# Performance work log

Hardware: AMD Instinct MI355X
Metric: run time of the kernel (lower is better)

## Reference

```python
import jax, jax.numpy as jnp
import numpy as np

N, K, H = 100000, 16, 128


def setup_inputs() -> dict:
    key = jax.random.key(0)
    ks = jax.random.split(key, 9)
    return {
        "p_init": jax.random.normal(ks[0], (N,), dtype=jnp.float32),
        "r_matrix": jax.random.normal(ks[1], (N, K, 5), dtype=jnp.float32),
        "w1": jax.random.normal(ks[2], (1 + 5, H), dtype=jnp.float32) * 0.1,
        "b1": jax.random.normal(ks[3], (H,), dtype=jnp.float32) * 0.1,
        "w2": jax.random.normal(ks[4], (H + 5, H), dtype=jnp.float32) * 0.05,
        "b2": jax.random.normal(ks[5], (H,), dtype=jnp.float32) * 0.05,
        "w3": jax.random.normal(ks[6], (H + 5, 1), dtype=jnp.float32) * 0.05,
        "b3": jax.random.normal(ks[7], (1,), dtype=jnp.float32) * 0.05,
        "indices_neigh_tri": jax.random.randint(ks[8], (N, K + 1), 0, N, dtype=jnp.int64),
    }


def _stage(f, neigh, r_matrix, w, b):
    # f: [N, C]; neigh: [N, K]; r_matrix: [N, K, 5]
    diff = f[:, None, :] - f[neigh]                      # [N, K, C]
    r_diff = jnp.concatenate([r_matrix, diff], axis=2)   # [N, K, 5+C]
    out = jnp.einsum('nkc,co->nko', r_diff, w) + b       # [N, K, O]
    return out.sum(axis=1)                               # [N, O]


def reference(p_init, r_matrix, w1, b1, w2, b2, w3, b3, indices_neigh_tri):
    neigh = indices_neigh_tri[:, 1:]                     # [N, K]
    f = p_init[:, None]                                  # [N, 1]
    f = jax.nn.relu(_stage(f, neigh, r_matrix, w1, b1))  # [N, H]
    f = jax.nn.relu(_stage(f, neigh, r_matrix, w2, b2))  # [N, H]
    logits = _stage(f, neigh, r_matrix, w3, b3).squeeze(-1)  # [N]
    return jax.nn.softmax(logits, axis=0)
```

## Files before the change

### kernel.cpp

```cpp
#include <hip/hip_runtime.h>
#include <hip/hip_bf16.h>
#include <hip/hip_fp16.h>


#define NN 100000
#define KK 16
#define HH 128

typedef _Float16 half8 __attribute__((ext_vector_type(8)));
typedef float f32x4 __attribute__((ext_vector_type(4)));
typedef float f32x2 __attribute__((ext_vector_type(2)));

__global__ __launch_bounds__(256) void prep_kernel(
    const float* __restrict__ p, const float* __restrict__ rmat,
    const int* __restrict__ idx, float* __restrict__ vv,
    unsigned int* __restrict__ gmk, float* __restrict__ pstot) {
  const int tid = threadIdx.x;
  if (blockIdx.x == 0 && tid == 0) { gmk[0] = 0u; pstot[0] = 0.f; }
  const int sub = tid & 3;
  const int n = blockIdx.x * 64 + (tid >> 2);
  if (n >= NN) return;
  const float4* rr = (const float4*)(rmat) + (size_t)n * 20;
  float t[5] = {0.f, 0.f, 0.f, 0.f, 0.f};
#pragma unroll
  for (int j = 0; j < 5; ++j) {
    const float4 q = rr[sub + 4 * j];
    t[(j + 0) % 5] += q.x;
    t[(j + 1) % 5] += q.y;
    t[(j + 2) % 5] += q.z;
    t[(j + 3) % 5] += q.w;
  }
  float rs[5];
#pragma unroll
  for (int c = 0; c < 5; ++c) {
    float v = t[c];
    v = (sub == 1) ? t[(c + 1) % 5] : v;
    v = (sub == 2) ? t[(c + 2) % 5] : v;
    v = (sub == 3) ? t[(c + 3) % 5] : v;
    rs[c] = v;
  }
  const int* nb = idx + (size_t)n * 17 + 1;
  float ps = 0.f;
#pragma unroll
  for (int k = 0; k < 4; ++k) ps += p[nb[sub * 4 + k]];
#pragma unroll
  for (int c = 0; c < 5; ++c) {
    rs[c] += __shfl_xor(rs[c], 1, 64);
    rs[c] += __shfl_xor(rs[c], 2, 64);
  }
  ps += __shfl_xor(ps, 1, 64);
  ps += __shfl_xor(ps, 2, 64);
  if (sub == 0) {
    float4 lo; lo.x = rs[0]; lo.y = rs[1]; lo.z = rs[2]; lo.w = rs[3];
    *(float4*)&vv[(size_t)n * 8] = lo;
  } else if (sub == 1) {
    float4 hi; hi.x = rs[4]; hi.y = 16.f * p[n] - ps; hi.z = 0.f; hi.w = 0.f;
    *(float4*)&vv[(size_t)n * 8 + 4] = hi;
  }
}

__global__ __launch_bounds__(256, 2) void gemm2_kernel(
    const float* __restrict__ vv, const float* __restrict__ w1,
    const float* __restrict__ b1, const float* __restrict__ w2,
    unsigned char* __restrict__ A8) {
  __shared__ __align__(16) _Float16 s_w1[6][128];
  __shared__ __align__(16) _Float16 s_b1[128];
  const int tid = threadIdx.x;
  if (tid < 128) {
#pragma unroll
    for (int c = 0; c < 6; ++c) s_w1[c][tid] = (_Float16)w1[c * HH + tid];
    s_b1[tid] = (_Float16)(16.f * b1[tid]);
  }
  const int lane = tid & 63;
  const int wgl = (blockIdx.x << 2) + (tid >> 6);
  const int colhalf = wgl & 1;
  const int strip0 = wgl >> 1;
  const int sstride = (gridDim.x << 2) >> 1;
  const int r16 = lane & 15;
  const int g16 = lane >> 4;

  half8 wfrag[4][4];
#pragma unroll
  for (int ct = 0; ct < 4; ++ct) {
#pragma unroll
    for (int kk = 0; kk < 4; ++kk) {
      const int hcol = colhalf * 64 + ct * 16 + r16;
#pragma unroll
      for (int e = 0; e < 8; ++e)
        wfrag[ct][kk][e] = (_Float16)w2[(size_t)(5 + kk * 32 + g16 * 8 + e) * HH + hcol];
    }
  }
  __syncthreads();

  for (int strip = strip0; strip < NN / 16; strip += sstride) {
    const int nbase = strip * 16;
    const float* vr = vv + (size_t)(nbase + r16) * 8;
    const float4 vlo = *(const float4*)vr;
    const float4 vhi = *(const float4*)(vr + 4);
    const _Float16 x0 = (_Float16)vlo.x, x1 = (_Float16)vlo.y,
                   x2 = (_Float16)vlo.z, x3 = (_Float16)vlo.w,
                   x4 = (_Float16)vhi.x, x5 = (_Float16)vhi.y;
    half8 xfrag[4];
#pragma unroll
    for (int kk = 0; kk < 4; ++kk) {
      const int off = kk * 32 + g16 * 8;
      half8 a = *(const half8*)&s_b1[off];
      const half8 w0 = *(const half8*)&s_w1[0][off];
      const half8 w1v = *(const half8*)&s_w1[1][off];
      const half8 w2v = *(const half8*)&s_w1[2][off];
      const half8 w3v = *(const half8*)&s_w1[3][off];
      const half8 w4v = *(const half8*)&s_w1[4][off];
      const half8 w5v = *(const half8*)&s_w1[5][off];
#pragma unroll
      for (int e = 0; e < 8; ++e) {
        _Float16 v = a[e] + w0[e] * x0 + w1v[e] * x1 + w2v[e] * x2
                   + w3v[e] * x3 + w4v[e] * x4 + w5v[e] * x5;
        a[e] = v > (_Float16)0.f ? v : (_Float16)0.f;
      }
      xfrag[kk] = a;
    }
    f32x4 acc[4] = {{0.f,0.f,0.f,0.f},{0.f,0.f,0.f,0.f},{0.f,0.f,0.f,0.f},{0.f,0.f,0.f,0.f}};
#pragma unroll
    for (int kk = 0; kk < 4; ++kk) {
#pragma unroll
      for (int ct = 0; ct < 4; ++ct)
        acc[ct] = __builtin_amdgcn_mfma_f32_16x16x32_f16(wfrag[ct][kk], xfrag[kk], acc[ct], 0, 0, 0);
    }
#pragma unroll
    for (int ct = 0; ct < 4; ++ct) {
      int packed = __builtin_amdgcn_cvt_pk_fp8_f32(acc[ct][0], acc[ct][1], 0, false);
      packed = __builtin_amdgcn_cvt_pk_fp8_f32(acc[ct][2], acc[ct][3], packed, true);
      *(int*)&A8[(size_t)(nbase + r16) * HH + colhalf * 64 + ct * 16 + g16 * 4] = packed;
    }
  }
}

#define REDUCE_PAIR(NBASE, AV0, AV1, DRAW)                                    \
  {                                                                           \
    f32x2 s0l = {0.f,0.f}, s0h = {0.f,0.f}, s1l = {0.f,0.f}, s1h = {0.f,0.f};\
    _Pragma("unroll")                                                         \
    for (int pp = 0; pp < 8; ++pp) {                                          \
      s0l -= __builtin_amdgcn_cvt_pk_f32_fp8(AV0[pp], false);                 \
      s0h -= __builtin_amdgcn_cvt_pk_f32_fp8(AV0[pp], true);                  \
      s1l -= __builtin_amdgcn_cvt_pk_f32_fp8(AV1[pp], false);                 \
      s1h -= __builtin_amdgcn_cvt_pk_f32_fp8(AV1[pp], true);                  \
    }                                                                         \
    {                                                                         \
      const int nd = (NBASE) + half;                                          \
      f32x2 dl = b2l + __builtin_amdgcn_cvt_pk_f32_fp8(DRAW, false);          \
      f32x2 dh = b2h + __builtin_amdgcn_cvt_pk_f32_fp8(DRAW, true);           \
      dl *= 16.f; dh *= 16.f;                                                 \
      const float* vr = vv + (size_t)nd * 8;                                  \
      _Pragma("unroll")                                                       \
      for (int j = 0; j < 5; ++j) {                                           \
        const float r = vr[j];                                                \
        dl += r * w2rl[j]; dh += r * w2rh[j];                                 \
      }                                                                       \
      if (half == 0) { s0l += dl; s0h += dh; }                                \
      else           { s1l += dl; s1h += dh; }                                \
    }                                                                         \
    s0l[0] += __shfl_xor(s0l[0], 32, 64); s0l[1] += __shfl_xor(s0l[1], 32, 64);\
    s0h[0] += __shfl_xor(s0h[0], 32, 64); s0h[1] += __shfl_xor(s0h[1], 32, 64);\
    s1l[0] += __shfl_xor(s1l[0], 32, 64); s1l[1] += __shfl_xor(s1l[1], 32, 64);\
    s1h[0] += __shfl_xor(s1h[0], 32, 64); s1h[1] += __shfl_xor(s1h[1], 32, 64);\
    float v0 = fmaxf(s0l[0], 0.f) * w3l[0] + fmaxf(s0l[1], 0.f) * w3l[1]      \
             + fmaxf(s0h[0], 0.f) * w3h[0] + fmaxf(s0h[1], 0.f) * w3h[1];     \
    float v1 = fmaxf(s1l[0], 0.f) * w3l[0] + fmaxf(s1l[1], 0.f) * w3l[1]      \
             + fmaxf(s1h[0], 0.f) * w3h[0] + fmaxf(s1h[1], 0.f) * w3h[1];     \
    _Pragma("unroll")                                                         \
    for (int off = 16; off > 0; off >>= 1) {                                  \
      v0 += __shfl_xor(v0, off, 64);                                          \
      v1 += __shfl_xor(v1, off, 64);                                          \
    }                                                                         \
    if (lane == 0) { sv[(NBASE)] = v0; sv[(NBASE) + 1] = v1; }                \
  }

__global__ __launch_bounds__(256) void gather2_kernel(
    const unsigned char* __restrict__ A8, const float* __restrict__ vv,
    const float* __restrict__ w2, const float* __restrict__ b2,
    const float* __restrict__ w3, const int* __restrict__ idx,
    float* __restrict__ sv) {
  const int lane = threadIdx.x & 63;
  const int half = lane >> 5;
  const int q = lane & 31;
  const int wid = (blockIdx.x << 2) + (threadIdx.x >> 6);
  const int nwaves = gridDim.x << 2;
  const f32x2 w3l = {w3[5 + 4 * q], w3[6 + 4 * q]};
  const f32x2 w3h = {w3[7 + 4 * q], w3[8 + 4 * q]};
  f32x2 w2rl[5], w2rh[5];
#pragma unroll
  for (int j = 0; j < 5; ++j) {
    w2rl[j] = *(const f32x2*)&w2[j * 128 + (q << 2)];
    w2rh[j] = *(const f32x2*)&w2[j * 128 + (q << 2) + 2];
  }
  const f32x2 b2l = *(const f32x2*)&b2[(q << 2)];
  const f32x2 b2h = *(const f32x2*)&b2[(q << 2) + 2];

  for (int t = wid; t < NN / 4; t += nwaves) {
    const int n = t * 4;
    const int* nb = idx + (size_t)n * 17 + 1;
    unsigned int avA[8], avB[8], avC[8], avD[8];
#pragma unroll
    for (int pp = 0; pp < 8; ++pp) {
      const int k = 2 * pp + half;
      avA[pp] = *(const unsigned int*)&A8[(size_t)nb[k]      * HH + (q << 2)];
      avB[pp] = *(const unsigned int*)&A8[(size_t)nb[17 + k] * HH + (q << 2)];
    }
    const unsigned int dAB = *(const unsigned int*)&A8[(size_t)(n + half) * HH + (q << 2)];
#pragma unroll
    for (int pp = 0; pp < 8; ++pp) {
      const int k = 2 * pp + half;
      avC[pp] = *(const unsigned int*)&A8[(size_t)nb[34 + k] * HH + (q << 2)];
      avD[pp] = *(const unsigned int*)&A8[(size_t)nb[51 + k] * HH + (q << 2)];
    }
    const unsigned int dCD = *(const unsigned int*)&A8[(size_t)(n + 2 + half) * HH + (q << 2)];
    REDUCE_PAIR(n, avA, avB, dAB)
    REDUCE_PAIR(n + 2, avC, avD, dCD)
  }
}

__device__ __forceinline__ unsigned int fkey(float f) {
  unsigned int b = __float_as_uint(f);
  return (b & 0x80000000u) ? ~b : (b | 0x80000000u);
}

__global__ __launch_bounds__(256) void stage3s_kernel(
    const float* __restrict__ sv, const float* __restrict__ vv,
    const float* __restrict__ w3, const float* __restrict__ b3,
    const int* __restrict__ idx, float* __restrict__ lg,
    unsigned int* __restrict__ gmk) {
  __shared__ float s[256];
  const int n = blockIdx.x * 256 + threadIdx.x;
  float t = -3.4e38f;
  if (n < NN) {
    t = 16.f * sv[n];
    const int* nb = idx + (size_t)n * 17 + 1;
#pragma unroll
    for (int k = 0; k < KK; ++k) t -= sv[nb[k]];
#pragma unroll
    for (int c = 0; c < 5; ++c) t += vv[(size_t)n * 8 + c] * w3[c];
    t += 16.f * b3[0];
    lg[n] = t;
  }
  s[threadIdx.x] = t; __syncthreads();
  for (int off = 128; off > 0; off >>= 1) {
    if (threadIdx.x < off) s[threadIdx.x] = fmaxf(s[threadIdx.x], s[threadIdx.x + off]);
    __syncthreads();
  }
  if (threadIdx.x == 0) atomicMax(gmk, fkey(s[0]));
}

__global__ __launch_bounds__(256) void expsum_kernel(
    const float* __restrict__ lg, const unsigned int* __restrict__ gmk,
    float* __restrict__ out, float* __restrict__ pstot) {
  __shared__ float s[256];
  const int tid = threadIdx.x;
  const unsigned int k = gmk[0];
  const float m = __uint_as_float((k & 0x80000000u) ? (k & 0x7FFFFFFFu) : ~k);
  float acc = 0.f;
  for (int i = blockIdx.x * 256 + tid; i < NN; i += 256 * 256) {
    float e = __expf(lg[i] - m);
    out[i] = e;
    acc += e;
  }
  s[tid] = acc; __syncthreads();
  for (int off = 128; off > 0; off >>= 1) {
    if (tid < off) s[tid] += s[tid + off];
    __syncthreads();
  }
  if (tid == 0) atomicAdd(pstot, s[0]);
}

__global__ __launch_bounds__(256) void scale_kernel(
    float* __restrict__ out, const float* __restrict__ pstot) {
  const int i = blockIdx.x * 256 + threadIdx.x;
  const float inv = 1.f / pstot[0];
  if (i < NN) out[i] *= inv;
}

extern "C" void kernel_launch(void* const* d_in, const int* in_sizes, int n_in,
                              void* d_out, int out_size, void* d_ws, size_t ws_size,
                              hipStream_t stream) {
  const float* p    = (const float*)d_in[0];
  const float* rmat = (const float*)d_in[1];
  const float* w1   = (const float*)d_in[2];
  const float* b1   = (const float*)d_in[3];
  const float* w2   = (const float*)d_in[4];
  const float* b2   = (const float*)d_in[5];
  const float* w3   = (const float*)d_in[6];
  const float* b3   = (const float*)d_in[7];
  const int*   idx  = (const int*)d_in[8];
  float* out = (float*)d_out;
  float* ws = (float*)d_ws;

  float* vv = ws;
  unsigned char* A8 = (unsigned char*)(ws + (size_t)NN * 8);
  float* sv  = (float*)(A8 + (size_t)NN * HH);
  float* lg  = sv + NN;
  unsigned int* gmk = (unsigned int*)(lg + NN);
  float* pstot = (float*)(gmk + 1);

  prep_kernel<<<(NN + 63) / 64, 256, 0, stream>>>(p, rmat, idx, vv, gmk, pstot);
  gemm2_kernel<<<1024, 256, 0, stream>>>(vv, w1, b1, w2, A8);
  gather2_kernel<<<2048, 256, 0, stream>>>(A8, vv, w2, b2, w3, idx, sv);
  stage3s_kernel<<<(NN + 255) / 256, 256, 0, stream>>>(sv, vv, w3, b3, idx, lg, gmk);
  expsum_kernel<<<256, 256, 0, stream>>>(lg, gmk, out, pstot);
  scale_kernel<<<(NN + 255) / 256, 256, 0, stream>>>(out, pstot);
}
```

Baseline: 82.96 us.

## Fuse softmax tail into one kernel with grid-wide spin barriers

Merges the logit, exp-sum and scale kernels into a single tail kernel that keeps each logit and exponent in registers. Two global atomic counters act as grid barriers to publish the max and the sum. This removes two launches and the round trip of logits and exponentials through global memory. The catch is that all 391 blocks must be co-resident, or the spin-wait deadlocks; this holds at this grid size on MI355X but is not guaranteed.

```diff
diff --git a/kernel.cpp b/kernel.cpp
--- a/kernel.cpp
+++ b/kernel.cpp
@@ -6,6 +6,7 @@
 #define NN 100000
 #define KK 16
 #define HH 128
+#define NBLK ((NN + 255) / 256)
 
 typedef _Float16 half8 __attribute__((ext_vector_type(8)));
 typedef float f32x4 __attribute__((ext_vector_type(4)));
@@ -14,9 +15,9 @@
 __global__ __launch_bounds__(256) void prep_kernel(
     const float* __restrict__ p, const float* __restrict__ rmat,
     const int* __restrict__ idx, float* __restrict__ vv,
-    unsigned int* __restrict__ gmk, float* __restrict__ pstot) {
+    unsigned int* __restrict__ sem) {
   const int tid = threadIdx.x;
-  if (blockIdx.x == 0 && tid == 0) { gmk[0] = 0u; pstot[0] = 0.f; }
+  if (blockIdx.x == 0 && tid < 4) sem[tid] = 0u;
   const int sub = tid & 3;
   const int n = blockIdx.x * 64 + (tid >> 2);
   if (n >= NN) return;
@@ -224,13 +225,15 @@
   return (b & 0x80000000u) ? ~b : (b | 0x80000000u);
 }
 
-__global__ __launch_bounds__(256) void stage3s_kernel(
+__global__ __launch_bounds__(256) void tail_kernel(
     const float* __restrict__ sv, const float* __restrict__ vv,
     const float* __restrict__ w3, const float* __restrict__ b3,
-    const int* __restrict__ idx, float* __restrict__ lg,
-    unsigned int* __restrict__ gmk) {
+    const int* __restrict__ idx, float* __restrict__ out,
+    unsigned int* __restrict__ sem) {
   __shared__ float s[256];
-  const int n = blockIdx.x * 256 + threadIdx.x;
+  __shared__ float sh_bcast;
+  const int tid = threadIdx.x;
+  const int n = blockIdx.x * 256 + tid;
   float t = -3.4e38f;
   if (n < NN) {
     t = 16.f * sv[n];
@@ -240,42 +243,38 @@
 #pragma unroll
     for (int c = 0; c < 5; ++c) t += vv[(size_t)n * 8 + c] * w3[c];
     t += 16.f * b3[0];
-    lg[n] = t;
-  }
-  s[threadIdx.x] = t; __syncthreads();
+  }
+  s[tid] = t; __syncthreads();
   for (int off = 128; off > 0; off >>= 1) {
-    if (threadIdx.x < off) s[threadIdx.x] = fmaxf(s[threadIdx.x], s[threadIdx.x + off]);
+    if (tid < off) s[tid] = fmaxf(s[tid], s[tid + off]);
     __syncthreads();
   }
-  if (threadIdx.x == 0) atomicMax(gmk, fkey(s[0]));
-}
-
-__global__ __launch_bounds__(256) void expsum_kernel(
-    const float* __restrict__ lg, const unsigned int* __restrict__ gmk,
-    float* __restrict__ out, float* __restrict__ pstot) {
-  __shared__ float s[256];
-  const int tid = threadIdx.x;
-  const unsigned int k = gmk[0];
-  const float m = __uint_as_float((k & 0x80000000u) ? (k & 0x7FFFFFFFu) : ~k);
-  float acc = 0.f;
-  for (int i = blockIdx.x * 256 + tid; i < NN; i += 256 * 256) {
-    float e = __expf(lg[i] - m);
-    out[i] = e;
-    acc += e;
-  }
-  s[tid] = acc; __syncthreads();
+  if (tid == 0) {
+    atomicMax(&sem[0], fkey(s[0]));
+    __threadfence();
+    atomicAdd(&sem[1], 1u);
+    while (atomicAdd(&sem[1], 0u) < (unsigned)NBLK) { __builtin_amdgcn_s_sleep(8); }
+    const unsigned int k = atomicAdd(&sem[0], 0u);
+    sh_bcast = __uint_as_float((k & 0x80000000u) ? (k & 0x7FFFFFFFu) : ~k);
+  }
+  __syncthreads();
+  const float m = sh_bcast;
+  const float e = (n < NN) ? __expf(t - m) : 0.f;
+  __syncthreads();
+  s[tid] = e; __syncthreads();
   for (int off = 128; off > 0; off >>= 1) {
     if (tid < off) s[tid] += s[tid + off];
     __syncthreads();
   }
-  if (tid == 0) atomicAdd(pstot, s[0]);
-}
-
-__global__ __launch_bounds__(256) void scale_kernel(
-    float* __restrict__ out, const float* __restrict__ pstot) {
-  const int i = blockIdx.x * 256 + threadIdx.x;
-  const float inv = 1.f / pstot[0];
-  if (i < NN) out[i] *= inv;
+  if (tid == 0) {
+    atomicAdd((float*)&sem[3], s[0]);
+    __threadfence();
+    atomicAdd(&sem[2], 1u);
+    while (atomicAdd(&sem[2], 0u) < (unsigned)NBLK) { __builtin_amdgcn_s_sleep(8); }
+    sh_bcast = 1.f / atomicAdd((float*)&sem[3], 0.f);
+  }
+  __syncthreads();
+  if (n < NN) out[n] = e * sh_bcast;
 }
 
 extern "C" void kernel_launch(void* const* d_in, const int* in_sizes, int n_in,
@@ -296,14 +295,10 @@
   float* vv = ws;
   unsigned char* A8 = (unsigned char*)(ws + (size_t)NN * 8);
   float* sv  = (float*)(A8 + (size_t)NN * HH);
-  float* lg  = sv + NN;
-  unsigned int* gmk = (unsigned int*)(lg + NN);
-  float* pstot = (float*)(gmk + 1);
-
-  prep_kernel<<<(NN + 63) / 64, 256, 0, stream>>>(p, rmat, idx, vv, gmk, pstot);
+  unsigned int* sem = (unsigned int*)(sv + NN);
+
+  prep_kernel<<<(NN + 63) / 64, 256, 0, stream>>>(p, rmat, idx, vv, sem);
   gemm2_kernel<<<1024, 256, 0, stream>>>(vv, w1, b1, w2, A8);
   gather2_kernel<<<2048, 256, 0, stream>>>(A8, vv, w2, b2, w3, idx, sv);
-  stage3s_kernel<<<(NN + 255) / 256, 256, 0, stream>>>(sv, vv, w3, b3, idx, lg, gmk);
-  expsum_kernel<<<256, 256, 0, stream>>>(lg, gmk, out, pstot);
-  scale_kernel<<<(NN + 255) / 256, 256, 0, stream>>>(out, pstot);
-}
+  tail_kernel<<<NBLK, 256, 0, stream>>>(sv, vv, w3, b3, idx, out, sem);
+}
```

After: 147.0 us. +77.3%, slower.
